# Kernel tuning notes

Measured on AMD Instinct MI355X. Metric: run time of the kernel, lower is better.

## Reference

```python
import jax, jax.numpy as jnp
import numpy as np

B, T, C = 8, 4096, 1024
NH = 64          # module sets self.n_head = dim_head = 64
HD = C // NH     # 16


def setup_inputs() -> dict:
    key = jax.random.key(0)
    ks = jax.random.split(key, 9)
    s = 1.0 / np.sqrt(C).astype(np.float32)
    x = jax.random.normal(ks[0], (B, T, C), jnp.float32)
    Wq = jax.random.normal(ks[1], (C, C), jnp.float32) * s
    bq = jax.random.normal(ks[2], (C,), jnp.float32) * 0.01
    Wk = jax.random.normal(ks[3], (C, C), jnp.float32) * s
    bk = jax.random.normal(ks[4], (C,), jnp.float32) * 0.01
    Wv = jax.random.normal(ks[5], (C, C), jnp.float32) * s
    bv = jax.random.normal(ks[6], (C,), jnp.float32) * 0.01
    Wp = jax.random.normal(ks[7], (C, C), jnp.float32) * s
    bp = jax.random.normal(ks[8], (C,), jnp.float32) * 0.01
    return {"x": x, "Wq": Wq, "bq": bq, "Wk": Wk, "bk": bk,
            "Wv": Wv, "bv": bv, "Wp": Wp, "bp": bp}


def _heads(t):
    # [B, T, C] -> [B, NH, T, HD]
    return t.reshape(B, T, NH, HD).transpose(0, 2, 1, 3)


def reference(x, Wq, bq, Wk, bk, Wv, bv, Wp, bp):
    # self-attention path: y = x; kv_mask=None (masked path is unreachable in source)
    q = _heads(x @ Wq.T + bq)
    k = _heads(x @ Wk.T + bk)
    v = _heads(x @ Wv.T + bv)
    q = jax.nn.softmax(q, axis=-1)
    k = jax.nn.softmax(k, axis=-1)
    k_cumsum = k.sum(axis=2, keepdims=True)               # [B, NH, 1, HD]
    D_inv = 1.0 / (q * k_cumsum).sum(axis=-1, keepdims=True)  # [B, NH, T, 1]
    context = jnp.einsum('bhtd,bhte->bhde', k, v)          # [B, NH, HD, HD]
    y = jnp.einsum('bhtd,bhde->bhte', q, context) * D_inv  # [B, NH, T, HD]
    y = y.transpose(0, 2, 1, 3).reshape(B, T, C)           # b h n d -> b n (h d)
    return y @ Wp.T + bp
```

## Files before the change

kernel.cpp:

```cpp
#include <hip/hip_runtime.h>
#include <stdint.h>


typedef __attribute__((ext_vector_type(8))) __bf16 bf16x8;
typedef __attribute__((ext_vector_type(4))) float f32x4;
typedef __attribute__((ext_vector_type(4))) unsigned int u32x4;
typedef __attribute__((ext_vector_type(4))) unsigned short u16x4;

#define AS1 __attribute__((address_space(1)))
#define AS3 __attribute__((address_space(3)))

__device__ __forceinline__ unsigned short f2bf(float f) {
  unsigned int u = __builtin_bit_cast(unsigned int, f);
  u += 0x7FFFu + ((u >> 16) & 1u);
  return (unsigned short)(u >> 16);
}

__device__ __forceinline__ void gl_lds16(const unsigned short* g, unsigned short* l) {
  __builtin_amdgcn_global_load_lds((const AS1 unsigned int*)g, (AS3 unsigned int*)l, 16, 0, 0);
}

__global__ __launch_bounds__(256)
void cvt_x(const float* __restrict__ src, unsigned short* __restrict__ dst, int n4) {
  int i = blockIdx.x * blockDim.x + threadIdx.x;
  const int stride = gridDim.x * blockDim.x;
  for (; i < n4; i += stride) {
    f32x4 v = *(const f32x4*)(src + (size_t)i * 4);
    u16x4 o;
    o.x = f2bf(v.x); o.y = f2bf(v.y); o.z = f2bf(v.z); o.w = f2bf(v.w);
    *(u16x4*)(dst + (size_t)i * 4) = o;
  }
}

__global__ __launch_bounds__(256)
void cvt_w(const float* __restrict__ w0, const float* __restrict__ w1,
           const float* __restrict__ w2, const float* __restrict__ w3,
           unsigned short* __restrict__ dst) {
  const int g = blockIdx.x * 256 + threadIdx.x;
  const int w = g >> 17;
  const int r = g & 131071;
  const int f = r >> 6;
  const int l = r & 63;
  const int n = (f >> 5) * 16 + (l & 15);
  const int k = (f & 31) * 32 + (l >> 4) * 8;
  const float* ws[4] = {w0, w1, w2, w3};
  const float* src = ws[w] + (size_t)n * 1024 + k;
  f32x4 v0 = *(const f32x4*)src;
  f32x4 v1 = *(const f32x4*)(src + 4);
  u16x4 a, b;
  a.x = f2bf(v0.x); a.y = f2bf(v0.y); a.z = f2bf(v0.z); a.w = f2bf(v0.w);
  b.x = f2bf(v1.x); b.y = f2bf(v1.y); b.z = f2bf(v1.z); b.w = f2bf(v1.w);
  unsigned short* o = dst + (size_t)g * 8;
  *(u16x4*)o = a;
  *(u16x4*)(o + 4) = b;
}

template<int KIND>
__global__ __launch_bounds__(256, 3)
void gemm_pipe(const unsigned short* __restrict__ A,
               const unsigned short* __restrict__ Wf,
               const float* __restrict__ b0, const float* __restrict__ b1,
               const float* __restrict__ b2,
               unsigned short* __restrict__ oq, unsigned short* __restrict__ okT,
               unsigned short* __restrict__ ovT, float* __restrict__ of)
{
  __shared__ __align__(16) unsigned short lds[12288];

  const int tid  = threadIdx.x;
  const int lane = tid & 63;
  const int wid  = tid >> 6;

  const int flat  = blockIdx.x;
  const int xcd   = flat & 7;
  const int i     = flat >> 3;
  const int bcg   = i >> 8;
  const int r     = i & 255;
  const int panel = r >> 3;
  const int c     = r & 7;
  const int brow  = (xcd * 32 + panel) * 128;
  const int bcol  = (bcg * 8 + c) * 128;

  const int srow = wid * 16 + (lane >> 2);
  const int scol = ((lane & 3) ^ ((lane >> 3) & 3)) << 3;
  const unsigned short* a_src = A + (size_t)(brow + srow) * 1024 + scol;
  unsigned short* Ldst = lds + wid * 512;

  const int wm = (wid >> 1) * 64;
  const int wn = (wid & 1) * 64;
  const int fr = lane & 15;
  const int fg = lane >> 4;
  const int aoff = (wm + fr) * 32 + ((fg ^ ((fr >> 1) & 3)) << 3);

  const unsigned short* wfp = Wf + ((size_t)((bcol + wn) >> 4) * 32) * 512 + lane * 8;

  const f32x4 fz = {0.f, 0.f, 0.f, 0.f};
  f32x4 acc[4][4];
  #pragma unroll
  for (int mt = 0; mt < 4; ++mt)
    #pragma unroll
    for (int nt = 0; nt < 4; ++nt) acc[mt][nt] = fz;

  auto stage = [&](int t, int buf) {
    unsigned short* d = Ldst + buf * 4096;
    gl_lds16(a_src + t * 32, d);
    gl_lds16(a_src + t * 32 + 65536, d + 2048);
  };
  auto loadB = [&](int t, bf16x8 (&dst)[4]) {
    #pragma unroll
    for (int nt = 0; nt < 4; ++nt)
      dst[nt] = __builtin_bit_cast(bf16x8,
        *(const u32x4*)(wfp + (size_t)t * 512 + (size_t)nt * 16384));
  };

  bf16x8 brgA[4], brgB[4];

  loadB(0, brgA);
  stage(0, 0); stage(1, 1); stage(2, 2);
  asm volatile("s_waitcnt vmcnt(4)" ::: "memory");
  __builtin_amdgcn_sched_barrier(0);
  __builtin_amdgcn_s_barrier();

  auto body = [&](int t, bf16x8 (&bc_)[4], bf16x8 (&bn_)[4]) {
    const unsigned short* Lb = lds + (t % 3) * 4096;
    bf16x8 af[4];
    #pragma unroll
    for (int mt = 0; mt < 4; ++mt)
      af[mt] = __builtin_bit_cast(bf16x8, *(const u32x4*)&Lb[aoff + mt * 512]);
    asm volatile("s_waitcnt lgkmcnt(0)" ::: "memory");
    __builtin_amdgcn_sched_barrier(0);
    __builtin_amdgcn_s_barrier();
    if (t + 3 < 32) stage(t + 3, t % 3);
    if (t + 1 < 32) loadB(t + 1, bn_);
    if (t <= 28)      asm volatile("s_waitcnt vmcnt(6)" ::: "memory");
    else if (t <= 30) asm volatile("s_waitcnt vmcnt(4)" ::: "memory");
    else              asm volatile("s_waitcnt vmcnt(0)" ::: "memory");
    __builtin_amdgcn_sched_barrier(0);
    __builtin_amdgcn_s_setprio(1);
    #pragma unroll
    for (int mt = 0; mt < 4; ++mt)
      #pragma unroll
      for (int nt = 0; nt < 4; ++nt)
        acc[mt][nt] = __builtin_amdgcn_mfma_f32_16x16x32_bf16(af[mt], bc_[nt], acc[mt][nt], 0, 0, 0);
    __builtin_amdgcn_s_setprio(0);
  };

  for (int t = 0; t < 32; t += 2) {
    body(t,     brgA, brgB);
    body(t + 1, brgB, brgA);
  }

  const int sec = (KIND == 0) ? (bcol >> 10) : 0;
  const float* bias = (KIND == 1) ? b0 : (sec == 0 ? b0 : (sec == 1 ? b1 : b2));

  #pragma unroll
  for (int nt = 0; nt < 4; ++nt) {
    const int n_glob = bcol + wn + nt * 16 + fr;
    const int nn = (KIND == 0) ? (n_glob & 1023) : n_glob;
    const float bv = bias[nn];
    #pragma unroll
    for (int mt = 0; mt < 4; ++mt) {
      const int m0 = brow + wm + mt * 16 + fg * 4;
      float vals[4];
      #pragma unroll
      for (int r2 = 0; r2 < 4; ++r2) vals[r2] = acc[mt][nt][r2] + bv;

      if (KIND == 0 && sec <= 1) {
        #pragma unroll
        for (int r2 = 0; r2 < 4; ++r2) {
          float e = __expf(vals[r2]);
          float sm = e;
          #pragma unroll
          for (int s = 1; s < 16; s <<= 1) sm += __shfl_xor(sm, s, 64);
          vals[r2] = e * __builtin_amdgcn_rcpf(sm);
        }
      }

      if (KIND == 1) {
        #pragma unroll
        for (int r2 = 0; r2 < 4; ++r2)
          of[(size_t)(m0 + r2) * 1024 + n_glob] = vals[r2];
      } else if (sec == 0) {
        #pragma unroll
        for (int r2 = 0; r2 < 4; ++r2)
          oq[(size_t)(m0 + r2) * 1024 + nn] = f2bf(vals[r2]);
      } else {
        unsigned short* o = (sec == 1) ? okT : ovT;
        const int bb = m0 >> 12;
        const int t0 = m0 & 4095;
        const int hh = nn >> 4;
        const int dd = nn & 15;
        u16x4 pk;
        pk.x = f2bf(vals[0]); pk.y = f2bf(vals[1]);
        pk.z = f2bf(vals[2]); pk.w = f2bf(vals[3]);
        *(u16x4*)&o[(((size_t)bb * 64 + hh) * 16 + dd) * 4096 + t0] = pk;
      }
    }
  }
}

__global__ __launch_bounds__(256)
void attn_kernel(const unsigned short* __restrict__ qb,
                 const unsigned short* __restrict__ kT,
                 const unsigned short* __restrict__ vT,
                 unsigned short* __restrict__ yb)
{
  const int pair = blockIdx.x;
  const int b    = pair >> 5;
  const int hp   = pair & 31;
  const int tid  = threadIdx.x;
  const int lane = tid & 63;
  const int wid  = tid >> 6;
  const int fr   = lane & 15;
  const int fg   = lane >> 4;

  const unsigned short* kT0 = kT + ((size_t)(b * 64 + hp * 2) * 16) * 4096;
  const unsigned short* vT0 = vT + ((size_t)(b * 64 + hp * 2) * 16) * 4096;
  const unsigned short* kT1 = kT0 + 16 * 4096;
  const unsigned short* vT1 = vT0 + 16 * 4096;

  const u32x4 uz = {0u, 0u, 0u, 0u};
  const f32x4 fz = {0.f, 0.f, 0.f, 0.f};
  const u32x4 uo = {0x3F803F80u, 0x3F803F80u, 0x3F803F80u, 0x3F803F80u};
  const bf16x8 ones = __builtin_bit_cast(bf16x8, uo);

  f32x4 cctx0 = fz, ckc0 = fz, cctx1 = fz, ckc1 = fz;
  #pragma unroll 2
  for (int t0 = wid * 1024; t0 < (wid + 1) * 1024; t0 += 32) {
    const size_t off = (size_t)fr * 4096 + t0 + fg * 8;
    bf16x8 ak0 = __builtin_bit_cast(bf16x8, *(const u32x4*)&kT0[off]);
    bf16x8 bv0 = __builtin_bit_cast(bf16x8, *(const u32x4*)&vT0[off]);
    bf16x8 ak1 = __builtin_bit_cast(bf16x8, *(const u32x4*)&kT1[off]);
    bf16x8 bv1 = __builtin_bit_cast(bf16x8, *(const u32x4*)&vT1[off]);
    cctx0 = __builtin_amdgcn_mfma_f32_16x16x32_bf16(ak0, bv0, cctx0, 0, 0, 0);
    ckc0  = __builtin_amdgcn_mfma_f32_16x16x32_bf16(ak0, ones, ckc0, 0, 0, 0);
    cctx1 = __builtin_amdgcn_mfma_f32_16x16x32_bf16(ak1, bv1, cctx1, 0, 0, 0);
    ckc1  = __builtin_amdgcn_mfma_f32_16x16x32_bf16(ak1, ones, ckc1, 0, 0, 0);
  }

  __shared__ float red[4][2][16][16];
  __shared__ float kcr[4][2][16];
  __shared__ float ctxf[2][16][16];
  __shared__ float kcf[2][16];

  #pragma unroll
  for (int r = 0; r < 4; ++r) {
    red[wid][0][fg * 4 + r][fr] = cctx0[r];
    red[wid][1][fg * 4 + r][fr] = cctx1[r];
  }
  if (fr == 0) {
    #pragma unroll
    for (int r = 0; r < 4; ++r) {
      kcr[wid][0][fg * 4 + r] = ckc0[r];
      kcr[wid][1][fg * 4 + r] = ckc1[r];
    }
  }
  __syncthreads();
  {
    const int h = tid >> 8;
    (void)h;
    const int d = (tid >> 4) & 15, e = tid & 15;
    #pragma unroll
    for (int hh = 0; hh < 2; ++hh)
      ctxf[hh][d][e] = red[0][hh][d][e] + red[1][hh][d][e] + red[2][hh][d][e] + red[3][hh][d][e];
    if (tid < 32) {
      const int hh = tid >> 4, dd = tid & 15;
      kcf[hh][dd] = kcr[0][hh][dd] + kcr[1][hh][dd] + kcr[2][hh][dd] + kcr[3][hh][dd];
    }
  }
  __syncthreads();

  bf16x8 bctx0 = __builtin_bit_cast(bf16x8, uz);
  bf16x8 bctx1 = __builtin_bit_cast(bf16x8, uz);
  bf16x8 bkc0  = __builtin_bit_cast(bf16x8, uz);
  bf16x8 bkc1  = __builtin_bit_cast(bf16x8, uz);
  if (fg < 2) {
    #pragma unroll
    for (int j = 0; j < 8; ++j) {
      const int d = fg * 8 + j;
      bctx0[j] = (__bf16)ctxf[0][d][fr];
      bkc0[j]  = (__bf16)kcf[0][d];
    }
  } else {
    #pragma unroll
    for (int j = 0; j < 8; ++j) {
      const int d = (fg - 2) * 8 + j;
      bctx1[j] = (__bf16)ctxf[1][d][fr];
      bkc1[j]  = (__bf16)kcf[1][d];
    }
  }

  const size_t cbase = (size_t)b * 4096 * 1024 + (size_t)hp * 32;

  for (int step = 0; step < 64; ++step) {
    const int t0 = step * 64 + wid * 16;
    bf16x8 af = __builtin_bit_cast(bf16x8,
        *(const u32x4*)&qb[cbase + (size_t)(t0 + fr) * 1024 + fg * 8]);
    f32x4 cy0 = __builtin_amdgcn_mfma_f32_16x16x32_bf16(af, bctx0, fz, 0, 0, 0);
    f32x4 cy1 = __builtin_amdgcn_mfma_f32_16x16x32_bf16(af, bctx1, fz, 0, 0, 0);
    f32x4 cd0 = __builtin_amdgcn_mfma_f32_16x16x32_bf16(af, bkc0,  fz, 0, 0, 0);
    f32x4 cd1 = __builtin_amdgcn_mfma_f32_16x16x32_bf16(af, bkc1,  fz, 0, 0, 0);
    #pragma unroll
    for (int r = 0; r < 4; ++r) {
      const int t = t0 + fg * 4 + r;
      const size_t o = cbase + (size_t)t * 1024;
      yb[o + fr]      = f2bf(cy0[r] * __builtin_amdgcn_rcpf(cd0[r]));
      yb[o + 16 + fr] = f2bf(cy1[r] * __builtin_amdgcn_rcpf(cd1[r]));
    }
  }
}

extern "C" void kernel_launch(void* const* d_in, const int* in_sizes, int n_in,
                              void* d_out, int out_size, void* d_ws, size_t ws_size,
                              hipStream_t stream)
{
  (void)in_sizes; (void)n_in; (void)out_size; (void)ws_size;
  const float* x  = (const float*)d_in[0];
  const float* Wq = (const float*)d_in[1];
  const float* bq = (const float*)d_in[2];
  const float* Wk = (const float*)d_in[3];
  const float* bk = (const float*)d_in[4];
  const float* Wv = (const float*)d_in[5];
  const float* bv = (const float*)d_in[6];
  const float* Wp = (const float*)d_in[7];
  const float* bp = (const float*)d_in[8];

  char* ws = (char*)d_ws;
  unsigned short* xb  = (unsigned short*)(ws);
  unsigned short* wb  = (unsigned short*)(ws + 67108864);
  unsigned short* qb  = (unsigned short*)(ws + 75497472);
  unsigned short* kTb = (unsigned short*)(ws + 142606336);
  unsigned short* vTb = (unsigned short*)(ws + 209715200);

  cvt_x<<<2048, 256, 0, stream>>>(x, xb, 33554432 / 4);
  cvt_w<<<2048, 256, 0, stream>>>(Wq, Wk, Wv, Wp, wb);

  gemm_pipe<0><<<6144, 256, 0, stream>>>(xb, wb, bq, bk, bv, qb, kTb, vTb, nullptr);

  attn_kernel<<<256, 256, 0, stream>>>(qb, kTb, vTb, xb );

  gemm_pipe<1><<<2048, 256, 0, stream>>>(xb , wb + 3145728, bp, bp, bp,
                                         nullptr, nullptr, nullptr, (float*)d_out);
}
```

Before: 462.7 us.

## Double GEMM K-step to 64 per barrier with larger LDS stages

The GEMM main loop now stages 64-wide K slices (two 32-wide halves) per LDS buffer and runs 16 iterations instead of 32. This halves the number of block barriers and LDS wait points. B fragments are prefetched in an even/odd register pair across the two halves. LDS usage doubles to 48KB per block, which may lower occupancy below the launch-bounds target of 3 blocks per CU.

New measurement: 453.5 us. 1.02x faster.

```diff
diff --git a/kernel.cpp b/kernel.cpp
--- a/kernel.cpp
+++ b/kernel.cpp
@@ -64,7 +64,7 @@
                unsigned short* __restrict__ oq, unsigned short* __restrict__ okT,
                unsigned short* __restrict__ ovT, float* __restrict__ of)
 {
-  __shared__ __align__(16) unsigned short lds[12288];
+  __shared__ __align__(16) unsigned short lds[24576];
 
   const int tid  = threadIdx.x;
   const int lane = tid & 63;
@@ -100,53 +100,67 @@
     #pragma unroll
     for (int nt = 0; nt < 4; ++nt) acc[mt][nt] = fz;
 
-  auto stage = [&](int t, int buf) {
-    unsigned short* d = Ldst + buf * 4096;
-    gl_lds16(a_src + t * 32, d);
-    gl_lds16(a_src + t * 32 + 65536, d + 2048);
+  auto stage = [&](int T, int sb) {
+    unsigned short* d = Ldst + sb * 8192;
+    const unsigned short* g = a_src + T * 64;
+    gl_lds16(g,              d);
+    gl_lds16(g + 65536,      d + 2048);
+    gl_lds16(g + 32,         d + 4096);
+    gl_lds16(g + 65536 + 32, d + 6144);
   };
-  auto loadB = [&](int t, bf16x8 (&dst)[4]) {
+  auto loadB = [&](int k32, bf16x8 (&dst)[4]) {
     #pragma unroll
     for (int nt = 0; nt < 4; ++nt)
       dst[nt] = __builtin_bit_cast(bf16x8,
-        *(const u32x4*)(wfp + (size_t)t * 512 + (size_t)nt * 16384));
+        *(const u32x4*)(wfp + (size_t)k32 * 512 + (size_t)nt * 16384));
   };
 
-  bf16x8 brgA[4], brgB[4];
-
-  loadB(0, brgA);
-  stage(0, 0); stage(1, 1); stage(2, 2);
-  asm volatile("s_waitcnt vmcnt(4)" ::: "memory");
+  bf16x8 bEven[4], bOdd[4];
+
+  stage(0, 0); stage(1, 1);
+  loadB(0, bEven);
+  asm volatile("s_waitcnt vmcnt(8)" ::: "memory");
   __builtin_amdgcn_sched_barrier(0);
   __builtin_amdgcn_s_barrier();
 
-  auto body = [&](int t, bf16x8 (&bc_)[4], bf16x8 (&bn_)[4]) {
-    const unsigned short* Lb = lds + (t % 3) * 4096;
-    bf16x8 af[4];
-    #pragma unroll
-    for (int mt = 0; mt < 4; ++mt)
-      af[mt] = __builtin_bit_cast(bf16x8, *(const u32x4*)&Lb[aoff + mt * 512]);
+  for (int T = 0; T < 16; ++T) {
+    const unsigned short* Lb = lds + (T % 3) * 8192;
+    bf16x8 af[8];
+    #pragma unroll
+    for (int mt = 0; mt < 4; ++mt) {
+      af[mt]     = __builtin_bit_cast(bf16x8, *(const u32x4*)&Lb[aoff + mt * 512]);
+      af[4 + mt] = __builtin_bit_cast(bf16x8, *(const u32x4*)&Lb[4096 + aoff + mt * 512]);
+    }
     asm volatile("s_waitcnt lgkmcnt(0)" ::: "memory");
     __builtin_amdgcn_sched_barrier(0);
-    __builtin_amdgcn_s_barrier();
-    if (t + 3 < 32) stage(t + 3, t % 3);
-    if (t + 1 < 32) loadB(t + 1, bn_);
-    if (t <= 28)      asm volatile("s_waitcnt vmcnt(6)" ::: "memory");
-    else if (t <= 30) asm volatile("s_waitcnt vmcnt(4)" ::: "memory");
-    else              asm volatile("s_waitcnt vmcnt(0)" ::: "memory");
+    if (T + 2 < 16) stage(T + 2, (T + 2) % 3);
+    loadB(2 * T + 1, bOdd);
+    if (T <= 13)      asm volatile("s_waitcnt vmcnt(8)" ::: "memory");
+    else              asm volatile("s_waitcnt vmcnt(4)" ::: "memory");
     __builtin_amdgcn_sched_barrier(0);
+    if (T < 15) __builtin_amdgcn_s_barrier();
+
     __builtin_amdgcn_s_setprio(1);
     #pragma unroll
     for (int mt = 0; mt < 4; ++mt)
       #pragma unroll
       for (int nt = 0; nt < 4; ++nt)
-        acc[mt][nt] = __builtin_amdgcn_mfma_f32_16x16x32_bf16(af[mt], bc_[nt], acc[mt][nt], 0, 0, 0);
+        acc[mt][nt] = __builtin_amdgcn_mfma_f32_16x16x32_bf16(af[mt], bEven[nt], acc[mt][nt], 0, 0, 0);
     __builtin_amdgcn_s_setprio(0);
-  };
-
-  for (int t = 0; t < 32; t += 2) {
-    body(t,     brgA, brgB);
-    body(t + 1, brgB, brgA);
+
+    if (T <= 14) loadB(2 * T + 2, bEven);
+    if (T <= 13)      asm volatile("s_waitcnt vmcnt(8)" ::: "memory");
+    else if (T == 14) asm volatile("s_waitcnt vmcnt(4)" ::: "memory");
+    else              asm volatile("s_waitcnt vmcnt(0)" ::: "memory");
+    __builtin_amdgcn_sched_barrier(0);
+
+    __builtin_amdgcn_s_setprio(1);
+    #pragma unroll
+    for (int mt = 0; mt < 4; ++mt)
+      #pragma unroll
+      for (int nt = 0; nt < 4; ++nt)
+        acc[mt][nt] = __builtin_amdgcn_mfma_f32_16x16x32_bf16(af[4 + mt], bOdd[nt], acc[mt][nt], 0, 0, 0);
+    __builtin_amdgcn_s_setprio(0);
   }
 
   const int sec = (KIND == 0) ? (bcol >> 10) : 0;
@@ -256,8 +270,6 @@
   }
   __syncthreads();
   {
-    const int h = tid >> 8;
-    (void)h;
     const int d = (tid >> 4) & 15, e = tid & 15;
     #pragma unroll
     for (int hh = 0; hh < 2; ++hh)
```
